# Optimization experiments

Measured on AMD Instinct MI355X. Metric: run time of the kernel, lower is better.

## Reference

```python
import jax, jax.numpy as jnp
import numpy as np
from jax import lax


def _lstm(x, h, c, W, U, b):
    # torch LSTM gate order: i, f, g, o; b = b_ih + b_hh combined
    g = x @ W.T + h @ U.T + b
    i, f, gg, o = jnp.split(g, 4, axis=-1)
    c2 = jax.nn.sigmoid(f) * c + jax.nn.sigmoid(i) * jnp.tanh(gg)
    h2 = jax.nn.sigmoid(o) * jnp.tanh(c2)
    return h2, c2


def _run_dir(x, mask, W, U, b):
    # packed-sequence semantics: state updates only where mask, outputs 0 at pad
    B = x.shape[0]
    Hh = U.shape[1]
    h0 = jnp.zeros((B, Hh), x.dtype)

    def step(carry, inp):
        h, c = carry
        xt, mt = inp
        h2, c2 = _lstm(xt, h, c, W, U, b)
        m = mt[:, None]
        h = jnp.where(m, h2, h)
        c = jnp.where(m, c2, c)
        return (h, c), jnp.where(m, h, jnp.zeros_like(h))

    (hf, cf), outs = lax.scan(step, (h0, h0), (jnp.swapaxes(x, 0, 1), mask.T))
    return jnp.swapaxes(outs, 0, 1), hf, cf  # (B,S,H), (B,H), (B,H)


def _forward(source, source_mask, target, target_mask, emb_src, emb_tgt,
             eW0f, eU0f, eb0f, eW0b, eU0b, eb0b,
             eW1f, eU1f, eb1f, eW1b, eU1b, eb1b,
             dW0, dU0, db0, dW1, dU1, db1, wW, wb):
    x = emb_src[source]  # (B,S,D)
    finals_h, finals_c = [], []
    enc_params = [(eW0f, eU0f, eb0f, eW0b, eU0b, eb0b),
                  (eW1f, eU1f, eb1f, eW1b, eU1b, eb1b)]
    for Wf, Uf, bf, Wb, Ub, bb in enc_params:
        of, hf, cf = _run_dir(x, source_mask, Wf, Uf, bf)
        # backward direction: reverse time; prefix mask becomes suffix, so the
        # masked-update scan exactly reproduces packed reverse-direction LSTM
        ob, hb, cb = _run_dir(x[:, ::-1], source_mask[:, ::-1], Wb, Ub, bb)
        ob = ob[:, ::-1]
        x = jnp.concatenate([of, ob], axis=-1)
        finals_h.append(jnp.concatenate([hf, hb], axis=-1))  # (B, 2H)
        finals_c.append(jnp.concatenate([cf, cb], axis=-1))

    # decoder initial state: per-layer concat of fwd/bwd encoder final states
    xt = emb_tgt[target]  # (B,T,D)

    def dstep(carry, inp):
        h1, c1, h2, c2 = carry
        t, mt = inp
        m = mt[:, None]
        nh1, nc1 = _lstm(t, h1, c1, dW0, dU0, db0)
        h1 = jnp.where(m, nh1, h1)
        c1 = jnp.where(m, nc1, c1)
        nh2, nc2 = _lstm(h1, h2, c2, dW1, dU1, db1)
        h2 = jnp.where(m, nh2, h2)
        c2 = jnp.where(m, nc2, c2)
        return (h1, c1, h2, c2), jnp.where(m, h2, jnp.zeros_like(h2))

    init = (finals_h[0], finals_c[0], finals_h[1], finals_c[1])
    _, outs = lax.scan(dstep, init, (jnp.swapaxes(xt, 0, 1), target_mask.T))
    outs = jnp.swapaxes(outs, 0, 1)  # (B,T,d_out)
    return jnp.einsum('btd,vd->btv', outs, wW) + wb  # (B,T,V)


def setup_inputs() -> dict:
    key = jax.random.key(0)
    ks = jax.random.split(key, 32)
    B, S, T, V, D, H = 32, 64, 65, 32000, 256, 512
    DO = 2 * H

    def p(i, shape):
        return jax.random.normal(ks[i], shape, dtype=jnp.float32) * 0.05

    source = jax.random.randint(ks[0], (B, S), 0, V + 1)
    target = jax.random.randint(ks[1], (B, T), 0, V + 1)
    # descending-sorted lengths -> sort/perm in the original is identity
    slen = jnp.sort(jax.random.randint(ks[2], (B,), 1, S + 1))[::-1]
    tlen = jnp.sort(jax.random.randint(ks[3], (B,), 1, T + 1))[::-1]
    source_mask = jnp.arange(S)[None, :] < slen[:, None]
    target_mask = jnp.arange(T)[None, :] < tlen[:, None]
    emb = p(4, (V + 1, D))
    return dict(
        source=source, source_mask=source_mask, target=target, target_mask=target_mask,
        emb_src=emb, emb_tgt=emb + 0.0,
        eW0f=p(5, (4 * H, D)), eU0f=p(6, (4 * H, H)), eb0f=p(7, (4 * H,)),
        eW0b=p(8, (4 * H, D)), eU0b=p(9, (4 * H, H)), eb0b=p(10, (4 * H,)),
        eW1f=p(11, (4 * H, 2 * H)), eU1f=p(12, (4 * H, H)), eb1f=p(13, (4 * H,)),
        eW1b=p(14, (4 * H, 2 * H)), eU1b=p(15, (4 * H, H)), eb1b=p(16, (4 * H,)),
        dW0=p(17, (4 * DO, D)), dU0=p(18, (4 * DO, DO)), db0=p(19, (4 * DO,)),
        dW1=p(20, (4 * DO, DO)), dU1=p(21, (4 * DO, DO)), db1=p(22, (4 * DO,)),
        wW=p(23, (V, DO)), wb=p(24, (V,)))


def reference(source, source_mask, target, target_mask, emb_src, emb_tgt,
              eW0f, eU0f, eb0f, eW0b, eU0b, eb0b,
              eW1f, eU1f, eb1f, eW1b, eU1b, eb1b,
              dW0, dU0, db0, dW1, dU1, db1, wW, wb):
    return _forward(source, source_mask, target, target_mask, emb_src, emb_tgt,
                    eW0f, eU0f, eb0f, eW0b, eU0b, eb0b,
                    eW1f, eU1f, eb1f, eW1b, eU1b, eb1b,
                    dW0, dU0, db0, dW1, dU1, db1, wW, wb)
```

## Files before the change

kernel.cpp:

```cpp
#include <hip/hip_runtime.h>

#define B_ 32
#define S_ 64
#define T_ 65
#define D_ 256
#define HE 512
#define HD 1024
#define VV 32000

typedef __attribute__((ext_vector_type(8))) short bf16x8;
typedef __attribute__((ext_vector_type(4))) float f32x4;
typedef __attribute__((ext_vector_type(4))) unsigned int u32x4;

__device__ inline unsigned short f2bf(float f) {
  unsigned int u = __float_as_uint(f);
  u += 0x7FFFu + ((u >> 16) & 1u);
  return (unsigned short)(u >> 16);
}
__device__ inline float sigmf(float x) { return 1.0f / (1.0f + __expf(-x)); }

#define MFMA16(a,b,c) __builtin_amdgcn_mfma_f32_16x16x32_bf16((a),(b),(c),0,0,0)

#define SLOT_STRIDE 32
__device__ inline void gbar_all(int* slots, int nblk, int e, int bid) {
  asm volatile("s_waitcnt vmcnt(0)" ::: "memory");
  __syncthreads();
  const int tid = threadIdx.x;
  if (tid == 0)
    __hip_atomic_store(&slots[bid * SLOT_STRIDE], e, __ATOMIC_RELAXED,
                       __HIP_MEMORY_SCOPE_AGENT);
  if (tid < nblk) {
    while (__hip_atomic_load(&slots[tid * SLOT_STRIDE], __ATOMIC_RELAXED,
                             __HIP_MEMORY_SCOPE_AGENT) < e)
      __builtin_amdgcn_s_sleep(2);
  }
  __syncthreads();
}

__device__ inline u32x4 ld16_sc(const void* p) {
  u32x4 r;
  asm volatile("global_load_dwordx4 %0, %1, off sc1"
               : "=v"(r)
               : "v"((unsigned long long)p)
               : "memory");
  return r;
}

__device__ inline void gl_lds16(const short* g, short* l) {
  __builtin_amdgcn_global_load_lds(
      (const __attribute__((address_space(1))) short*)g,
      (__attribute__((address_space(3))) short*)l, 16, 0, 0);
}

__device__ inline int swz(int row, int col, int LD) {
  return row * LD + ((((col >> 3) ^ (row & 7)) << 3) | (col & 7));
}
template <int LD>
__device__ inline void stage1a(short* lds, const short* src) {
  const int tid = threadIdx.x;
  constexpr int NPT = LD / 64;
  u32x4 t[NPT];
#pragma unroll
  for (int i = 0; i < NPT; i++)
    t[i] = ld16_sc(src + ((size_t)(i * 256 + tid)) * 8);
  asm volatile("s_waitcnt vmcnt(0)" ::: "memory");
  __builtin_amdgcn_sched_barrier(0);
#pragma unroll
  for (int i = 0; i < NPT; i++) {
    int o = (i * 256 + tid) * 8;
    *(u32x4*)(lds + swz(o / LD, o % LD, LD)) = t[i];
  }
}
__device__ inline void stage2a(short* lds1, const short* s1, short* lds2,
                               const short* s2) {
  const int tid = threadIdx.x;
  u32x4 t1[16], t2[16];
#pragma unroll
  for (int i = 0; i < 16; i++)
    t1[i] = ld16_sc(s1 + ((size_t)(i * 256 + tid)) * 8);
#pragma unroll
  for (int i = 0; i < 16; i++)
    t2[i] = ld16_sc(s2 + ((size_t)(i * 256 + tid)) * 8);
  asm volatile("s_waitcnt vmcnt(16)" ::: "memory");
  __builtin_amdgcn_sched_barrier(0);
#pragma unroll
  for (int i = 0; i < 16; i++) {
    int o = (i * 256 + tid) * 8;
    *(u32x4*)(lds1 + swz(o / HD, o % HD, HD)) = t1[i];
  }
  asm volatile("s_waitcnt vmcnt(0)" ::: "memory");
  __builtin_amdgcn_sched_barrier(0);
#pragma unroll
  for (int i = 0; i < 16; i++) {
    int o = (i * 256 + tid) * 8;
    *(u32x4*)(lds2 + swz(o / HD, o % HD, HD)) = t2[i];
  }
}

__device__ inline int mask_dtype(const unsigned char* m) {
  unsigned b0 = m[0], b1 = m[1], b2 = m[2], b3 = m[3], b4 = m[4];
  if (b0 == 1 && b1 == 1) return 0;
  if (b0 == 1) {
    if (b4 == 1) return 1;
    if (b4 == 0 && m[8] == 1) return 2;
    return 1;
  }
  if (b0 == 0x80 && b1 == 0x3F) return 4;
  if (b0 == 0x00 && b1 == 0x3C) return 5;
  if (b2 == 0x80 && b3 == 0x3F) return 3;
  return 1;
}
__device__ inline int mask_val(const unsigned char* m, int dt, int i) {
  switch (dt) {
    case 0: return m[i] != 0;
    case 1: return ((const int*)m)[i] != 0;
    case 2: return ((const long long*)m)[i] != 0;
    case 3: return ((const float*)m)[i] != 0.0f;
    default: return ((const unsigned short*)m)[i] != 0;
  }
}
__global__ void k_masks(const unsigned char* msrc, const unsigned char* mtgt,
                        signed char* o_src, signed char* o_tgt) {
  const unsigned char* m = blockIdx.x ? mtgt : msrc;
  signed char* o = blockIdx.x ? o_tgt : o_src;
  int n = blockIdx.x ? (B_ * T_) : (B_ * S_);
  int dt = mask_dtype(m);
  for (int i = threadIdx.x; i < n; i += blockDim.x)
    o[i] = (signed char)mask_val(m, dt, i);
}

struct CvtJobs {
  const float* src[13];
  short* dst[13];
  int n4[13];
};
__global__ __launch_bounds__(256) void k_convert(CvtJobs jb) {
  int j = blockIdx.y;
  const float4* s = (const float4*)jb.src[j];
  ushort4* d = (ushort4*)jb.dst[j];
  int n4 = jb.n4[j];
  for (int i = blockIdx.x * blockDim.x + threadIdx.x; i < n4;
       i += gridDim.x * blockDim.x) {
    float4 v = s[i];
    ushort4 o;
    o.x = f2bf(v.x); o.y = f2bf(v.y); o.z = f2bf(v.z); o.w = f2bf(v.w);
    d[i] = o;
  }
}

__global__ __launch_bounds__(256) void k_gather(const int* sids, const int* tids,
                                                const float* es, const float* et,
                                                short* Xs, short* Xt) {
  int job = blockIdx.y;
  int rows = job ? (B_ * T_) : (B_ * S_);
  const int* ids = job ? tids : sids;
  const float* emb = job ? et : es;
  ushort4* X = (ushort4*)(job ? Xt : Xs);
  int total = rows * (D_ / 4);
  for (int i = blockIdx.x * blockDim.x + threadIdx.x; i < total;
       i += gridDim.x * blockDim.x) {
    int row = i >> 6;
    int c4 = i & 63;
    long id = ids[row];
    float4 v = ((const float4*)(emb + id * (long)D_))[c4];
    ushort4 o;
    o.x = f2bf(v.x); o.y = f2bf(v.y); o.z = f2bf(v.z); o.w = f2bf(v.w);
    X[(long)row * 64 + c4] = o;
  }
}

__global__ __launch_bounds__(256) void k_gemm(const short* __restrict__ A,
                                              const short* __restrict__ Bw,
                                              const float* __restrict__ bias,
                                              float* __restrict__ Cf,
                                              int M_out, int N, int K) {
  __shared__ short As[128 * 32];
  __shared__ short Bs[128 * 32];
  const int tid = threadIdx.x;
  const int wave = tid >> 6, lane = tid & 63;
  const int wm = wave >> 1, wn = wave & 1;
  const int r16 = lane & 15, kb = lane >> 4;
  const long m0 = (long)blockIdx.y * 128;
  const long n0 = (long)blockIdx.x * 128;

  const int c0 = wave * 128 + lane, c1 = c0 + 64;
  const int rA0 = c0 >> 2, kA0 = (c0 & 3) * 8;
  const int rA1 = c1 >> 2, kA1 = (c1 & 3) * 8;
  short* lA0 = As + (size_t)(wave * 128) * 8;
  short* lA1 = As + (size_t)(wave * 128 + 64) * 8;
  short* lB0 = Bs + (size_t)(wave * 128) * 8;
  short* lB1 = Bs + (size_t)(wave * 128 + 64) * 8;

  f32x4 acc[4][4];
#pragma unroll
  for (int i = 0; i < 4; i++)
#pragma unroll
    for (int j = 0; j < 4; j++) acc[i][j] = (f32x4){0.f, 0.f, 0.f, 0.f};

  for (int kt = 0; kt < K; kt += 32) {
    __syncthreads();
    gl_lds16(A + (m0 + rA0) * K + kt + kA0, lA0);
    gl_lds16(A + (m0 + rA1) * K + kt + kA1, lA1);
    gl_lds16(Bw + (n0 + rA0) * K + kt + kA0, lB0);
    gl_lds16(Bw + (n0 + rA1) * K + kt + kA1, lB1);
    __syncthreads();
    bf16x8 av[4], bv[4];
#pragma unroll
    for (int i = 0; i < 4; i++)
      av[i] = *(const bf16x8*)(As + (wm * 64 + i * 16 + r16) * 32 + kb * 8);
#pragma unroll
    for (int j = 0; j < 4; j++)
      bv[j] = *(const bf16x8*)(Bs + (wn * 64 + j * 16 + r16) * 32 + kb * 8);
#pragma unroll
    for (int i = 0; i < 4; i++)
#pragma unroll
      for (int j = 0; j < 4; j++) acc[i][j] = MFMA16(av[i], bv[j], acc[i][j]);
  }
#pragma unroll
  for (int j = 0; j < 4; j++) {
    long gc = n0 + wn * 64 + j * 16 + r16;
    float bb = bias ? bias[gc] : 0.f;
#pragma unroll
    for (int i = 0; i < 4; i++) {
      long gr0 = m0 + wm * 64 + i * 16 + kb * 4;
#pragma unroll
      for (int r = 0; r < 4; r++) {
        long gr = gr0 + r;
        if (gr < M_out) Cf[gr * N + gc] = acc[i][j][r] + bb;
      }
    }
  }
}

__global__ __launch_bounds__(256) void k_enc_persist(
    const short* __restrict__ Wf, const short* __restrict__ Wb_,
    short* __restrict__ H, const float* __restrict__ Pf,
    const float* __restrict__ Pb, short* __restrict__ Outb, int outLD,
    int outOffDir, float* __restrict__ Cfin,
    const signed char* __restrict__ msk, int* slots) {
  const int dir = blockIdx.y;
  const short* W = dir ? Wb_ : Wf;
  const float* P = dir ? Pb : Pf;
  int* slotsD = slots + dir * 32 * SLOT_STRIDE;
  const int q = threadIdx.x >> 6, lane = threadIdx.x & 63;
  const int r16 = lane & 15, kb = lane >> 4;
  const int n = q * HE + blockIdx.x * 16 + r16;
  const short* wr = W + (size_t)n * HE;
  const int bb = threadIdx.x >> 3;
  const int cp = threadIdx.x & 7;
  const int j0 = blockIdx.x * 16 + 2 * cp;
  __shared__ short h_lds[32 * HE];
  __shared__ float g_lds[4][2][16][17];
  float creg0 = 0.f, creg1 = 0.f;

  for (int s = 0; s < S_; ++s) {
    const int t = dir ? (S_ - 1 - s) : s;
    const int rp = s & 1;
    const short* Ar = H + ((size_t)rp * 2 + dir) * (B_ * HE);
    short* Hw = H + ((size_t)(rp ^ 1) * 2 + dir) * (B_ * HE);

    const float* pr = P + (size_t)(bb * S_ + t) * (4 * HE);
    float2 pv[4];
#pragma unroll
    for (int g = 0; g < 4; g++) pv[g] = *(const float2*)(pr + g * HE + j0);
    bool valid = msk[bb * S_ + t] != 0;

    __syncthreads();
    stage1a<HE>(h_lds, Ar);
    __syncthreads();

    f32x4 acc0 = (f32x4){0.f, 0.f, 0.f, 0.f};
    f32x4 acc1 = (f32x4){0.f, 0.f, 0.f, 0.f};
#pragma unroll 8
    for (int k = kb * 8; k < HE; k += 32) {
      bf16x8 bv = *(const bf16x8*)(wr + k);
      bf16x8 a0 = *(const bf16x8*)(h_lds + swz(r16, k, HE));
      bf16x8 a1 = *(const bf16x8*)(h_lds + swz(16 + r16, k, HE));
      acc0 = MFMA16(a0, bv, acc0);
      acc1 = MFMA16(a1, bv, acc1);
    }
#pragma unroll
    for (int r = 0; r < 4; r++) {
      g_lds[q][0][kb * 4 + r][r16] = acc0[r];
      g_lds[q][1][kb * 4 + r][r16] = acc1[r];
    }
    __syncthreads();
    {
      const int mt = bb >> 4, br = bb & 15;
      float h2v[2];
#pragma unroll
      for (int cc = 0; cc < 2; ++cc) {
        float g0 = g_lds[0][mt][br][2 * cp + cc] + (cc ? pv[0].y : pv[0].x);
        float g1 = g_lds[1][mt][br][2 * cp + cc] + (cc ? pv[1].y : pv[1].x);
        float g2 = g_lds[2][mt][br][2 * cp + cc] + (cc ? pv[2].y : pv[2].x);
        float g3 = g_lds[3][mt][br][2 * cp + cc] + (cc ? pv[3].y : pv[3].x);
        float co = cc ? creg1 : creg0;
        float c2 = sigmf(g1) * co + sigmf(g0) * tanhf(g2);
        float h2 = sigmf(g3) * tanhf(c2);
        if (valid) { if (cc) creg1 = c2; else creg0 = c2; }
        h2v[cc] = h2;
      }
      unsigned short o0 = valid ? f2bf(h2v[0])
                                : (unsigned short)h_lds[swz(bb, j0, HE)];
      unsigned short o1 = valid ? f2bf(h2v[1])
                                : (unsigned short)h_lds[swz(bb, j0 + 1, HE)];
      unsigned int hv = (unsigned int)o0 | ((unsigned int)o1 << 16);
      __hip_atomic_store((unsigned int*)(Hw + bb * HE + j0), hv,
                         __ATOMIC_RELAXED, __HIP_MEMORY_SCOPE_AGENT);
      if (Outb) {
        unsigned int ov = valid ? hv : 0u;
        *(unsigned int*)(Outb + (size_t)(bb * S_ + t) * outLD +
                         outOffDir * dir + j0) = ov;
      }
    }
    if (s < S_ - 1) gbar_all(slotsD, 32, s + 1, blockIdx.x);
  }
  Cfin[(size_t)(dir * B_ + bb) * HE + j0] = creg0;
  Cfin[(size_t)(dir * B_ + bb) * HE + j0 + 1] = creg1;
}

__global__ __launch_bounds__(256) void k_dec_persist(
    const short* __restrict__ dU0b, const short* __restrict__ dW1b,
    const short* __restrict__ dU1b, short* __restrict__ H1,
    short* __restrict__ H2, const float* __restrict__ Q0,
    const float* __restrict__ db1f, const float* __restrict__ dC1i,
    const float* __restrict__ dC2i, short* __restrict__ douts,
    const signed char* __restrict__ msk, int* slots) {
  const int role = blockIdx.y;
  const int bid = role * 64 + blockIdx.x;
  const int q = threadIdx.x >> 6, lane = threadIdx.x & 63;
  const int r16 = lane & 15, kb = lane >> 4;
  const int n = q * HD + blockIdx.x * 16 + r16;
  const int bb = threadIdx.x >> 3;
  const int cp = threadIdx.x & 7;
  const int j0 = blockIdx.x * 16 + 2 * cp;
  __shared__ short h_lds1[32 * HD];
  __shared__ short h_lds2[32 * HD];
  __shared__ float g_lds[4][2][16][17];
  const float* Ci = role ? dC2i : dC1i;
  float creg0 = Ci[(size_t)bb * HD + j0];
  float creg1 = Ci[(size_t)bb * HD + j0 + 1];
  const short* w0 = dU0b + (size_t)n * HD;
  const short* w1 = dW1b + (size_t)n * HD;
  const short* w2 = dU1b + (size_t)n * HD;

  for (int k = 0; k <= T_; ++k) {
    if (role == 0 && k <= T_ - 1) {
      const int t = k, rp = k & 1;
      const short* Ar = H1 + (size_t)rp * (B_ * HD);
      short* Hw = H1 + (size_t)(rp ^ 1) * (B_ * HD);
      const float* pr = Q0 + (size_t)(bb * T_ + t) * (4 * HD);
      float2 pv[4];
#pragma unroll
      for (int g = 0; g < 4; g++) pv[g] = *(const float2*)(pr + g * HD + j0);
      bool valid = msk[bb * T_ + t] != 0;
      __syncthreads();
      stage1a<HD>(h_lds1, Ar);
      __syncthreads();
      f32x4 acc0 = (f32x4){0.f, 0.f, 0.f, 0.f};
      f32x4 acc1 = (f32x4){0.f, 0.f, 0.f, 0.f};
#pragma unroll 8
      for (int kk = kb * 8; kk < HD; kk += 32) {
        bf16x8 bv = *(const bf16x8*)(w0 + kk);
        bf16x8 a0 = *(const bf16x8*)(h_lds1 + swz(r16, kk, HD));
        bf16x8 a1 = *(const bf16x8*)(h_lds1 + swz(16 + r16, kk, HD));
        acc0 = MFMA16(a0, bv, acc0);
        acc1 = MFMA16(a1, bv, acc1);
      }
#pragma unroll
      for (int r = 0; r < 4; r++) {
        g_lds[q][0][kb * 4 + r][r16] = acc0[r];
        g_lds[q][1][kb * 4 + r][r16] = acc1[r];
      }
      __syncthreads();
      {
        const int mt = bb >> 4, br = bb & 15;
        float h2v[2];
#pragma unroll
        for (int cc = 0; cc < 2; ++cc) {
          float g0 = g_lds[0][mt][br][2 * cp + cc] + (cc ? pv[0].y : pv[0].x);
          float g1 = g_lds[1][mt][br][2 * cp + cc] + (cc ? pv[1].y : pv[1].x);
          float g2 = g_lds[2][mt][br][2 * cp + cc] + (cc ? pv[2].y : pv[2].x);
          float g3 = g_lds[3][mt][br][2 * cp + cc] + (cc ? pv[3].y : pv[3].x);
          float co = cc ? creg1 : creg0;
          float c2 = sigmf(g1) * co + sigmf(g0) * tanhf(g2);
          float h2 = sigmf(g3) * tanhf(c2);
          if (valid) { if (cc) creg1 = c2; else creg0 = c2; }
          h2v[cc] = h2;
        }
        unsigned short o0 = valid ? f2bf(h2v[0])
                                  : (unsigned short)h_lds1[swz(bb, j0, HD)];
        unsigned short o1 = valid ? f2bf(h2v[1])
                                  : (unsigned short)h_lds1[swz(bb, j0 + 1, HD)];
        unsigned int hv = (unsigned int)o0 | ((unsigned int)o1 << 16);
        __hip_atomic_store((unsigned int*)(Hw + bb * HD + j0), hv,
                           __ATOMIC_RELAXED, __HIP_MEMORY_SCOPE_AGENT);
      }
    } else if (role == 1 && k >= 1) {
      const int t = k - 1, rp = t & 1;
      const short* X = H1 + (size_t)(k & 1) * (B_ * HD);
      const short* Ar2 = H2 + (size_t)rp * (B_ * HD);
      short* Hw = H2 + (size_t)(rp ^ 1) * (B_ * HD);
      float2 pv[4];
#pragma unroll
      for (int g = 0; g < 4; g++) pv[g] = *(const float2*)(db1f + g * HD + j0);
      bool valid = msk[bb * T_ + t] != 0;
      __syncthreads();
      stage2a(h_lds1, X, h_lds2, Ar2);
      __syncthreads();
      f32x4 acc0 = (f32x4){0.f, 0.f, 0.f, 0.f};
      f32x4 acc1 = (f32x4){0.f, 0.f, 0.f, 0.f};
#pragma unroll 4
      for (int kk = kb * 8; kk < HD; kk += 32) {
        bf16x8 bv1 = *(const bf16x8*)(w1 + kk);
        bf16x8 a0 = *(const bf16x8*)(h_lds1 + swz(r16, kk, HD));
        bf16x8 a1 = *(const bf16x8*)(h_lds1 + swz(16 + r16, kk, HD));
        acc0 = MFMA16(a0, bv1, acc0);
        acc1 = MFMA16(a1, bv1, acc1);
        bf16x8 bv2 = *(const bf16x8*)(w2 + kk);
        bf16x8 b0 = *(const bf16x8*)(h_lds2 + swz(r16, kk, HD));
        bf16x8 b1 = *(const bf16x8*)(h_lds2 + swz(16 + r16, kk, HD));
        acc0 = MFMA16(b0, bv2, acc0);
        acc1 = MFMA16(b1, bv2, acc1);
      }
#pragma unroll
      for (int r = 0; r < 4; r++) {
        g_lds[q][0][kb * 4 + r][r16] = acc0[r];
        g_lds[q][1][kb * 4 + r][r16] = acc1[r];
      }
      __syncthreads();
      {
        const int mt = bb >> 4, br = bb & 15;
        float h2v[2];
#pragma unroll
        for (int cc = 0; cc < 2; ++cc) {
          float g0 = g_lds[0][mt][br][2 * cp + cc] + (cc ? pv[0].y : pv[0].x);
          float g1 = g_lds[1][mt][br][2 * cp + cc] + (cc ? pv[1].y : pv[1].x);
          float g2 = g_lds[2][mt][br][2 * cp + cc] + (cc ? pv[2].y : pv[2].x);
          float g3 = g_lds[3][mt][br][2 * cp + cc] + (cc ? pv[3].y : pv[3].x);
          float co = cc ? creg1 : creg0;
          float c2 = sigmf(g1) * co + sigmf(g0) * tanhf(g2);
          float h2 = sigmf(g3) * tanhf(c2);
          if (valid) { if (cc) creg1 = c2; else creg0 = c2; }
          h2v[cc] = h2;
        }
        unsigned short o0 = valid ? f2bf(h2v[0])
                                  : (unsigned short)h_lds2[swz(bb, j0, HD)];
        unsigned short o1 = valid ? f2bf(h2v[1])
                                  : (unsigned short)h_lds2[swz(bb, j0 + 1, HD)];
        unsigned int hv = (unsigned int)o0 | ((unsigned int)o1 << 16);
        __hip_atomic_store((unsigned int*)(Hw + bb * HD + j0), hv,
                           __ATOMIC_RELAXED, __HIP_MEMORY_SCOPE_AGENT);
        *(unsigned int*)(douts + (size_t)(bb * T_ + t) * HD + j0) =
            valid ? hv : 0u;
      }
    }
    if (k < T_) gbar_all(slots, 128, k + 1, bid);
  }
}

__global__ __launch_bounds__(256) void k_decinit(const short* h0, const float* c0,
                                                 const short* h1, const float* c1f,
                                                 short* dh1, float* dc1,
                                                 short* dh2, float* dc2) {
  int i = blockIdx.x * 256 + threadIdx.x;
  if (i < B_ * HD) {
    int b = i >> 10, nn = i & 1023, d = nn >> 9, jj = nn & 511;
    int src = (d * B_ + b) * HE + jj;
    dh1[i] = h0[src];
    dc1[i] = c0[src];
    dh2[i] = h1[src];
    dc2[i] = c1f[src];
  }
}

extern "C" void kernel_launch(void* const* d_in, const int* in_sizes, int n_in,
                              void* d_out, int out_size, void* d_ws, size_t ws_size,
                              hipStream_t stream) {
  const int* src = (const int*)d_in[0];
  const unsigned char* msrc = (const unsigned char*)d_in[1];
  const int* tgt = (const int*)d_in[2];
  const unsigned char* mtgt = (const unsigned char*)d_in[3];
  const float* emb_s = (const float*)d_in[4];
  const float* emb_t = (const float*)d_in[5];
  const float* eW0f = (const float*)d_in[6];
  const float* eU0f = (const float*)d_in[7];
  const float* eb0f = (const float*)d_in[8];
  const float* eW0b = (const float*)d_in[9];
  const float* eU0b = (const float*)d_in[10];
  const float* eb0b = (const float*)d_in[11];
  const float* eW1f = (const float*)d_in[12];
  const float* eU1f = (const float*)d_in[13];
  const float* eb1f = (const float*)d_in[14];
  const float* eW1b = (const float*)d_in[15];
  const float* eU1b = (const float*)d_in[16];
  const float* eb1b = (const float*)d_in[17];
  const float* dW0 = (const float*)d_in[18];
  const float* dU0 = (const float*)d_in[19];
  const float* db0 = (const float*)d_in[20];
  const float* dW1 = (const float*)d_in[21];
  const float* dU1 = (const float*)d_in[22];
  const float* db1 = (const float*)d_in[23];
  const float* wW = (const float*)d_in[24];
  const float* wb = (const float*)d_in[25];
  (void)n_in; (void)in_sizes; (void)out_size; (void)ws_size;

  short* douts = (short*)d_ws;
  short* wW_b = (short*)((char*)d_ws + (size_t)2176 * 1024 * 2);

  char* po = (char*)d_out;
  size_t off = 0;
  auto alloc = [&](size_t bytes) -> char* {
    char* p = po + off;
    off += (bytes + 255) & ~(size_t)255;
    return p;
  };
  const size_t szW[12] = {
      (size_t)2048 * 256 * 2,  (size_t)2048 * 512 * 2,
      (size_t)2048 * 256 * 2,  (size_t)2048 * 512 * 2,
      (size_t)2048 * 1024 * 2, (size_t)2048 * 512 * 2,
      (size_t)2048 * 1024 * 2, (size_t)2048 * 512 * 2,
      (size_t)4096 * 256 * 2,  (size_t)4096 * 1024 * 2,
      (size_t)4096 * 1024 * 2, (size_t)4096 * 1024 * 2};
  short* Wb[12];
  for (int i = 0; i < 12; i++) Wb[i] = (short*)alloc(szW[i]);
  short* eW0f_b = Wb[0], *eU0f_b = Wb[1], *eW0b_b = Wb[2], *eU0b_b = Wb[3];
  short* eW1f_b = Wb[4], *eU1f_b = Wb[5], *eW1b_b = Wb[6], *eU1b_b = Wb[7];
  short* dW0_b = Wb[8], *dU0_b = Wb[9], *dW1_b = Wb[10], *dU1_b = Wb[11];
  short* Xs_b = (short*)alloc((size_t)2048 * 256 * 2);
  short* Xt_b = (short*)alloc((size_t)2176 * 256 * 2);
  short* X1_b = (short*)alloc((size_t)2048 * 1024 * 2);
  char* uni = alloc((size_t)2176 * 4096 * 4);
  float* P0f = (float*)uni;
  float* P0b = P0f + (size_t)2048 * 2048;
  float* P1f = (float*)uni;
  float* P1b = P1f + (size_t)2048 * 2048;
  float* Q0 = (float*)uni;
  char* zero_begin = po + off;
  int* slots_e0 = (int*)alloc(2 * 32 * SLOT_STRIDE * 4);
  int* slots_e1 = (int*)alloc(2 * 32 * SLOT_STRIDE * 4);
  int* slots_d = (int*)alloc(128 * SLOT_STRIDE * 4);
  short* encH0 = (short*)alloc((size_t)2 * 2 * B_ * HE * 2);
  short* encH1 = (short*)alloc((size_t)2 * 2 * B_ * HE * 2);
  size_t zero_bytes = (size_t)((po + off) - zero_begin);
  float* Cfin0 = (float*)alloc((size_t)2 * B_ * HE * 4);
  float* Cfin1 = (float*)alloc((size_t)2 * B_ * HE * 4);
  short* dH1 = (short*)alloc((size_t)2 * B_ * HD * 2);
  short* dH2 = (short*)alloc((size_t)2 * B_ * HD * 2);
  float* dC1f = (float*)alloc((size_t)B_ * HD * 4);
  float* dC2f = (float*)alloc((size_t)B_ * HD * 4);
  signed char* msk_s = (signed char*)alloc(B_ * S_);
  signed char* msk_t = (signed char*)alloc(B_ * T_);

  (void)hipMemsetAsync(douts, 0, (size_t)2176 * 1024 * 2, stream);
  (void)hipMemsetAsync(zero_begin, 0, zero_bytes, stream);
  k_masks<<<dim3(2), dim3(256), 0, stream>>>(msrc, mtgt, msk_s, msk_t);
  CvtJobs jb;
  const float* srcs[13] = {eW0f, eU0f, eW0b, eU0b, eW1f, eU1f,
                           eW1b, eU1b, dW0, dU0, dW1, dU1, wW};
  short* dsts[13] = {Wb[0], Wb[1], Wb[2], Wb[3], Wb[4], Wb[5],
                     Wb[6], Wb[7], Wb[8], Wb[9], Wb[10], Wb[11], wW_b};
  int ns[13] = {2048 * 256, 2048 * 512, 2048 * 256, 2048 * 512,
                2048 * 1024, 2048 * 512, 2048 * 1024, 2048 * 512,
                4096 * 256, 4096 * 1024, 4096 * 1024, 4096 * 1024, VV * 1024};
  for (int i = 0; i < 13; i++) { jb.src[i] = srcs[i]; jb.dst[i] = dsts[i]; jb.n4[i] = ns[i] / 4; }
  k_convert<<<dim3(1024, 13), 256, 0, stream>>>(jb);
  k_gather<<<dim3(544, 2), 256, 0, stream>>>(src, tgt, emb_s, emb_t, Xs_b, Xt_b);

  k_gemm<<<dim3(16, 16), 256, 0, stream>>>(Xs_b, eW0f_b, eb0f, P0f,
                                           2048, 2048, 256);
  k_gemm<<<dim3(16, 16), 256, 0, stream>>>(Xs_b, eW0b_b, eb0b, P0b,
                                           2048, 2048, 256);

  k_enc_persist<<<dim3(32, 2), 256, 0, stream>>>(
      eU0f_b, eU0b_b, encH0, P0f, P0b, X1_b, 1024, 512, Cfin0, msk_s, slots_e0);

  k_gemm<<<dim3(16, 16), 256, 0, stream>>>(X1_b, eW1f_b, eb1f, P1f,
                                           2048, 2048, 1024);
  k_gemm<<<dim3(16, 16), 256, 0, stream>>>(X1_b, eW1b_b, eb1b, P1b,
                                           2048, 2048, 1024);

  k_enc_persist<<<dim3(32, 2), 256, 0, stream>>>(
      eU1f_b, eU1b_b, encH1, P1f, P1b, (short*)nullptr, 0, 0, Cfin1, msk_s,
      slots_e1);

  k_decinit<<<dim3(128), 256, 0, stream>>>(encH0, Cfin0, encH1, Cfin1,
                                           dH1, dC1f, dH2, dC2f);

  k_gemm<<<dim3(32, 17), 256, 0, stream>>>(Xt_b, dW0_b, db0, Q0,
                                           2176, 4096, 256);

  k_dec_persist<<<dim3(64, 2), 256, 0, stream>>>(
      dU0_b, dW1_b, dU1_b, dH1, dH2, Q0, db1, dC1f, dC2f, douts, msk_t,
      slots_d);

  k_gemm<<<dim3(250, 17), 256, 0, stream>>>(douts, wW_b, wb, (float*)d_out,
                                            B_ * T_, VV, 1024);
}
```

Measured before the change: 1.903 ms.

## Replace decoder global barrier with per-role epoch flags and 4-deep H1 ring

The persistent decoder kernel no longer has all 128 blocks meet at a global barrier every step. Layer-0 blocks now publish per-block epoch counters and wait only on their own layer plus layer-1 progress three steps back. Layer-1 blocks wait on their own layer and on layer-0's output for the step, and prefetch the next H1 into LDS right after signalling. The H1 buffer becomes a 4-slot ring so layer 0 can run ahead of layer 1, at the cost of more subtle ordering correctness and extra memory.

```diff
diff --git a/kernel.cpp b/kernel.cpp
--- a/kernel.cpp
+++ b/kernel.cpp
@@ -22,6 +22,38 @@
 #define MFMA16(a,b,c) __builtin_amdgcn_mfma_f32_16x16x32_bf16((a),(b),(c),0,0,0)
 
 #define SLOT_STRIDE 32
+__device__ inline void sig_epoch(int* slot, int e) {
+  asm volatile("s_waitcnt vmcnt(0)" ::: "memory");
+  __syncthreads();
+  if (threadIdx.x == 0)
+    __hip_atomic_store(slot, e, __ATOMIC_RELAXED, __HIP_MEMORY_SCOPE_AGENT);
+}
+__device__ inline void waitg(int* slots, int cnt, int need) {
+  const int tid = threadIdx.x;
+  if (need > 0 && tid < cnt) {
+    while (__hip_atomic_load(&slots[tid * SLOT_STRIDE], __ATOMIC_RELAXED,
+                             __HIP_MEMORY_SCOPE_AGENT) < need)
+      __builtin_amdgcn_s_sleep(2);
+  }
+  __syncthreads();
+}
+__device__ inline void waitg2(int* sA, int nA, int* sB, int nB) {
+  const int tid = threadIdx.x;
+  if (tid < 64) {
+    if (nA > 0) {
+      while (__hip_atomic_load(&sA[tid * SLOT_STRIDE], __ATOMIC_RELAXED,
+                               __HIP_MEMORY_SCOPE_AGENT) < nA)
+        __builtin_amdgcn_s_sleep(2);
+    }
+  } else if (tid < 128) {
+    if (nB > 0) {
+      while (__hip_atomic_load(&sB[(tid - 64) * SLOT_STRIDE], __ATOMIC_RELAXED,
+                               __HIP_MEMORY_SCOPE_AGENT) < nB)
+        __builtin_amdgcn_s_sleep(2);
+    }
+  }
+  __syncthreads();
+}
 __device__ inline void gbar_all(int* slots, int nblk, int e, int bid) {
   asm volatile("s_waitcnt vmcnt(0)" ::: "memory");
   __syncthreads();
@@ -69,31 +101,6 @@
   for (int i = 0; i < NPT; i++) {
     int o = (i * 256 + tid) * 8;
     *(u32x4*)(lds + swz(o / LD, o % LD, LD)) = t[i];
-  }
-}
-__device__ inline void stage2a(short* lds1, const short* s1, short* lds2,
-                               const short* s2) {
-  const int tid = threadIdx.x;
-  u32x4 t1[16], t2[16];
-#pragma unroll
-  for (int i = 0; i < 16; i++)
-    t1[i] = ld16_sc(s1 + ((size_t)(i * 256 + tid)) * 8);
-#pragma unroll
-  for (int i = 0; i < 16; i++)
-    t2[i] = ld16_sc(s2 + ((size_t)(i * 256 + tid)) * 8);
-  asm volatile("s_waitcnt vmcnt(16)" ::: "memory");
-  __builtin_amdgcn_sched_barrier(0);
-#pragma unroll
-  for (int i = 0; i < 16; i++) {
-    int o = (i * 256 + tid) * 8;
-    *(u32x4*)(lds1 + swz(o / HD, o % HD, HD)) = t1[i];
-  }
-  asm volatile("s_waitcnt vmcnt(0)" ::: "memory");
-  __builtin_amdgcn_sched_barrier(0);
-#pragma unroll
-  for (int i = 0; i < 16; i++) {
-    int o = (i * 256 + tid) * 8;
-    *(u32x4*)(lds2 + swz(o / HD, o % HD, HD)) = t2[i];
   }
 }
 
@@ -326,35 +333,35 @@
     const float* __restrict__ db1f, const float* __restrict__ dC1i,
     const float* __restrict__ dC2i, short* __restrict__ douts,
     const signed char* __restrict__ msk, int* slots) {
+  int* e0 = slots;
+  int* e1 = slots + 64 * SLOT_STRIDE;
   const int role = blockIdx.y;
-  const int bid = role * 64 + blockIdx.x;
+  const int bx = blockIdx.x;
   const int q = threadIdx.x >> 6, lane = threadIdx.x & 63;
   const int r16 = lane & 15, kb = lane >> 4;
-  const int n = q * HD + blockIdx.x * 16 + r16;
+  const int n = q * HD + bx * 16 + r16;
   const int bb = threadIdx.x >> 3;
   const int cp = threadIdx.x & 7;
-  const int j0 = blockIdx.x * 16 + 2 * cp;
+  const int j0 = bx * 16 + 2 * cp;
   __shared__ short h_lds1[32 * HD];
   __shared__ short h_lds2[32 * HD];
   __shared__ float g_lds[4][2][16][17];
   const float* Ci = role ? dC2i : dC1i;
   float creg0 = Ci[(size_t)bb * HD + j0];
   float creg1 = Ci[(size_t)bb * HD + j0 + 1];
-  const short* w0 = dU0b + (size_t)n * HD;
-  const short* w1 = dW1b + (size_t)n * HD;
-  const short* w2 = dU1b + (size_t)n * HD;
-
-  for (int k = 0; k <= T_; ++k) {
-    if (role == 0 && k <= T_ - 1) {
-      const int t = k, rp = k & 1;
-      const short* Ar = H1 + (size_t)rp * (B_ * HD);
-      short* Hw = H1 + (size_t)(rp ^ 1) * (B_ * HD);
+
+  if (role == 0) {
+    const short* w0 = dU0b + (size_t)n * HD;
+    for (int k = 0; k < T_; ++k) {
+      waitg2(e0, k, e1, k - 3);
+      const int t = k;
+      const short* Ar = H1 + (size_t)(k % 4) * (B_ * HD);
+      short* Hw = H1 + (size_t)((k + 1) % 4) * (B_ * HD);
       const float* pr = Q0 + (size_t)(bb * T_ + t) * (4 * HD);
       float2 pv[4];
 #pragma unroll
       for (int g = 0; g < 4; g++) pv[g] = *(const float2*)(pr + g * HD + j0);
       bool valid = msk[bb * T_ + t] != 0;
-      __syncthreads();
       stage1a<HD>(h_lds1, Ar);
       __syncthreads();
       f32x4 acc0 = (f32x4){0.f, 0.f, 0.f, 0.f};
@@ -396,18 +403,23 @@
         __hip_atomic_store((unsigned int*)(Hw + bb * HD + j0), hv,
                            __ATOMIC_RELAXED, __HIP_MEMORY_SCOPE_AGENT);
       }
-    } else if (role == 1 && k >= 1) {
-      const int t = k - 1, rp = t & 1;
-      const short* X = H1 + (size_t)(k & 1) * (B_ * HD);
-      const short* Ar2 = H2 + (size_t)rp * (B_ * HD);
-      short* Hw = H2 + (size_t)(rp ^ 1) * (B_ * HD);
-      float2 pv[4];
-#pragma unroll
-      for (int g = 0; g < 4; g++) pv[g] = *(const float2*)(db1f + g * HD + j0);
+      sig_epoch(&e0[bx * SLOT_STRIDE], k + 1);
+    }
+  } else {
+    const short* w1 = dW1b + (size_t)n * HD;
+    const short* w2 = dU1b + (size_t)n * HD;
+    float2 pvB[4];
+#pragma unroll
+    for (int g = 0; g < 4; g++) pvB[g] = *(const float2*)(db1f + g * HD + j0);
+    waitg(e0, 64, 1);
+    stage1a<HD>(h_lds1, H1 + (size_t)1 * (B_ * HD));
+    for (int k = 1; k <= T_; ++k) {
+      waitg(e1, 64, k - 1);
+      const int t = k - 1;
       bool valid = msk[bb * T_ + t] != 0;
+      stage1a<HD>(h_lds2, H2 + (size_t)((k + 1) & 1) * (B_ * HD));
       __syncthreads();
-      stage2a(h_lds1, X, h_lds2, Ar2);
-      __syncthreads();
+      short* Hw = H2 + (size_t)(k & 1) * (B_ * HD);
       f32x4 acc0 = (f32x4){0.f, 0.f, 0.f, 0.f};
       f32x4 acc1 = (f32x4){0.f, 0.f, 0.f, 0.f};
 #pragma unroll 4
@@ -434,10 +446,10 @@
         float h2v[2];
 #pragma unroll
         for (int cc = 0; cc < 2; ++cc) {
-          float g0 = g_lds[0][mt][br][2 * cp + cc] + (cc ? pv[0].y : pv[0].x);
-          float g1 = g_lds[1][mt][br][2 * cp + cc] + (cc ? pv[1].y : pv[1].x);
-          float g2 = g_lds[2][mt][br][2 * cp + cc] + (cc ? pv[2].y : pv[2].x);
-          float g3 = g_lds[3][mt][br][2 * cp + cc] + (cc ? pv[3].y : pv[3].x);
+          float g0 = g_lds[0][mt][br][2 * cp + cc] + (cc ? pvB[0].y : pvB[0].x);
+          float g1 = g_lds[1][mt][br][2 * cp + cc] + (cc ? pvB[1].y : pvB[1].x);
+          float g2 = g_lds[2][mt][br][2 * cp + cc] + (cc ? pvB[2].y : pvB[2].x);
+          float g3 = g_lds[3][mt][br][2 * cp + cc] + (cc ? pvB[3].y : pvB[3].x);
           float co = cc ? creg1 : creg0;
           float c2 = sigmf(g1) * co + sigmf(g0) * tanhf(g2);
           float h2 = sigmf(g3) * tanhf(c2);
@@ -454,8 +466,12 @@
         *(unsigned int*)(douts + (size_t)(bb * T_ + t) * HD + j0) =
             valid ? hv : 0u;
       }
-    }
-    if (k < T_) gbar_all(slots, 128, k + 1, bid);
+      sig_epoch(&e1[bx * SLOT_STRIDE], k);
+      if (k < T_) {
+        waitg(e0, 64, k + 1);
+        stage1a<HD>(h_lds1, H1 + (size_t)((k + 1) % 4) * (B_ * HD));
+      }
+    }
   }
 }
 
@@ -545,7 +561,7 @@
   size_t zero_bytes = (size_t)((po + off) - zero_begin);
   float* Cfin0 = (float*)alloc((size_t)2 * B_ * HE * 4);
   float* Cfin1 = (float*)alloc((size_t)2 * B_ * HE * 4);
-  short* dH1 = (short*)alloc((size_t)2 * B_ * HD * 2);
+  short* dH1 = (short*)alloc((size_t)4 * B_ * HD * 2);
   short* dH2 = (short*)alloc((size_t)2 * B_ * HD * 2);
   float* dC1f = (float*)alloc((size_t)B_ * HD * 4);
   float* dC2f = (float*)alloc((size_t)B_ * HD * 4);
```

Measured after the change: 1.895 ms, median of 2. Within noise of the previous version (-0.4%).
